# Optimization experiments

Measured on AMD Instinct MI355X. Metric: run time of the kernel, lower is better.

## Reference

```python
import jax, jax.numpy as jnp
import numpy as np

IN_F = 2
DIM_H = 64
DT = 0.02          # step_size
INTENSITY = 40.0   # Poisson rate multiplier
RATE = jnp.array([10.0, 1.0], dtype=jnp.float32)  # Gamma rates per feature


def _xavier(key, fan_in, fan_out):
    lim = float(np.sqrt(6.0 / (fan_in + fan_out)))
    return jax.random.uniform(key, (fan_in, fan_out), minval=-lim, maxval=lim, dtype=jnp.float32)


def setup_inputs() -> dict:
    key = jax.random.key(0)
    k0, k1, k2 = jax.random.split(key, 3)
    Nsim, steps = 100000, 200
    z0 = jax.random.normal(k0, (Nsim, IN_F), dtype=jnp.float32)
    W1 = _xavier(k1, IN_F, DIM_H)
    b1 = jnp.zeros((DIM_H,), dtype=jnp.float32)
    W2 = _xavier(k2, DIM_H, IN_F)
    b2 = jnp.zeros((IN_F,), dtype=jnp.float32)
    diffusion = jnp.float32(1.0)
    return {"z0": z0, "W1": W1, "b1": b1, "W2": W2, "b2": b2,
            "diffusion": diffusion, "Nsim": Nsim, "steps": steps}


def _drift(x, W1, b1, W2, b2):
    # MLP: Linear(2,64) -> tanh -> Linear(64,2)
    h = jnp.tanh(x @ W1 + b1)
    return h @ W2 + b2


def reference(z0, W1, b1, W2, b2, diffusion, Nsim, steps):
    sqrt_dt = jnp.float32(np.sqrt(DT))
    n = z0.shape[0]

    def step(state, key):
        kp, kn, kg = jax.random.split(key, 3)
        # Poisson(intensity*dt) jump counts, shape [N,1]
        pois = jax.random.poisson(kp, INTENSITY * DT, (n, 1)).astype(jnp.float32)
        a = jnp.broadcast_to(pois, (n, IN_F))  # Gamma concentration per feature
        # Gamma(conc=pois, rate=RATE); conc==0 -> sample is exactly 0
        g = jax.random.gamma(kg, jnp.maximum(a, 1.0), dtype=jnp.float32) / RATE
        jump = jnp.where(a > 0, g, 0.0)
        noise = jax.random.normal(kn, (n, IN_F), dtype=jnp.float32)
        new_state = (state
                     + _drift(state, W1, b1, W2, b2) * DT
                     + diffusion * sqrt_dt * noise
                     + jump)
        return new_state, new_state

    keys = jax.random.split(jax.random.key(42), steps)
    _, path = jax.lax.scan(step, z0, keys)            # [steps, N, F]
    path = jnp.concatenate([z0[None], path], axis=0)   # [steps+1, N, F]
    return jnp.transpose(path, (1, 0, 2))              # [N, steps+1, F]
```

## Files before the change

kernel.cpp:

```cpp
#include <hip/hip_runtime.h>
#include <cstdint>
#include <cmath>

#define DEVINL __device__ __forceinline__

struct U2 { uint32_t a, b; };
typedef float v2f __attribute__((ext_vector_type(2)));

DEVINL uint32_t rotl32(uint32_t x, uint32_t r){ return (x << r) | (x >> (32u - r)); }

DEVINL U2 tf(uint32_t k0, uint32_t k1, uint32_t x0, uint32_t x1){
  const uint32_t k2 = k0 ^ k1 ^ 0x1BD11BDAu;
  x0 += k0; x1 += k1;
#define TFR(r) { x0 += x1; x1 = rotl32(x1,(r)); x1 ^= x0; }
  TFR(13) TFR(15) TFR(26) TFR(6)  x0 += k1; x1 += k2 + 1u;
  TFR(17) TFR(29) TFR(16) TFR(24) x0 += k2; x1 += k0 + 2u;
  TFR(13) TFR(15) TFR(26) TFR(6)  x0 += k0; x1 += k1 + 3u;
  TFR(17) TFR(29) TFR(16) TFR(24) x0 += k1; x1 += k2 + 4u;
  TFR(13) TFR(15) TFR(26) TFR(6)  x0 += k2; x1 += k0 + 5u;
#undef TFR
  U2 r; r.a = x0; r.b = x1; return r;
}

DEVINL uint32_t pbits(uint32_t k0, uint32_t k1, uint32_t idx){
  U2 r = tf(k0, k1, 0u, idx);
  return r.a ^ r.b;
}

DEVINL float u01(uint32_t bits){
  return __uint_as_float((bits >> 9) | 0x3F800000u) - 1.0f;
}

DEVINL float xla_logf(float xin){
  float xf = fmaxf(__uint_as_float(0x00800000u), xin);
  uint32_t ib = __float_as_uint(xf);
  float e = (float)((int)(ib >> 23) - 126);
  float x = __uint_as_float((ib & 0x807fffffu) | 0x3f000000u);
  bool m = x < 0.707106781186547524f;
  float t = m ? x : 0.0f;
  x = __fsub_rn(x, 1.0f);
  if (m) e = __fsub_rn(e, 1.0f);
  x = __fadd_rn(x, t);
  float z = __fmul_rn(x, x);
  float y = 7.0376836292e-2f;
  y = fmaf(y, x, -1.1514610310e-1f);
  y = fmaf(y, x,  1.1676998740e-1f);
  y = fmaf(y, x, -1.2420140846e-1f);
  y = fmaf(y, x,  1.4249322787e-1f);
  y = fmaf(y, x, -1.6668057665e-1f);
  y = fmaf(y, x,  2.0000714765e-1f);
  y = fmaf(y, x, -2.4999993993e-1f);
  y = fmaf(y, x,  3.3333331174e-1f);
  y = __fmul_rn(y, x);
  y = __fmul_rn(y, z);
  y = fmaf(e, -2.12194440e-4f, y);
  y = fmaf(z, -0.5f, y);
  x = __fadd_rn(x, y);
  x = fmaf(e, 0.693359375f, x);
  if (xin == 0.0f) x = __uint_as_float(0xff800000u);
  return x;
}

DEVINL float xla_log1pf(float v){
  float av = fabsf(v);
  if (av < 1e-4f) return __fmul_rn(__fadd_rn(__fmul_rn(-0.5f, v), 1.0f), v);
  return xla_logf(__fadd_rn(v, 1.0f));
}

DEVINL float erfinv32(float x){
  float xx = __fmul_rn(x, x);
  float w = -xla_log1pf(-xx);
  float p;
  if (w < 5.0f){
    float ww = __fsub_rn(w, 2.5f);
    p = 2.81022636e-08f;
    p = __fadd_rn( 3.43273939e-07f, __fmul_rn(p, ww));
    p = __fadd_rn(-3.5233877e-06f,  __fmul_rn(p, ww));
    p = __fadd_rn(-4.39150654e-06f, __fmul_rn(p, ww));
    p = __fadd_rn( 0.00021858087f,  __fmul_rn(p, ww));
    p = __fadd_rn(-0.00125372503f,  __fmul_rn(p, ww));
    p = __fadd_rn(-0.00417768164f,  __fmul_rn(p, ww));
    p = __fadd_rn( 0.246640727f,    __fmul_rn(p, ww));
    p = __fadd_rn( 1.50140941f,     __fmul_rn(p, ww));
  } else {
    float ww = __fsub_rn(sqrtf(w), 3.0f);
    p = -0.000200214257f;
    p = __fadd_rn( 0.000100950558f, __fmul_rn(p, ww));
    p = __fadd_rn( 0.00134934322f,  __fmul_rn(p, ww));
    p = __fadd_rn(-0.00367342844f,  __fmul_rn(p, ww));
    p = __fadd_rn( 0.00573950773f,  __fmul_rn(p, ww));
    p = __fadd_rn(-0.0076224613f,   __fmul_rn(p, ww));
    p = __fadd_rn( 0.00943887047f,  __fmul_rn(p, ww));
    p = __fadd_rn( 1.00167406f,     __fmul_rn(p, ww));
    p = __fadd_rn( 2.83297682f,     __fmul_rn(p, ww));
  }
  return __fmul_rn(p, x);
}

#define SQRT2F (__uint_as_float(0x3FB504F3u))
#define NLOF   (__uint_as_float(0xBF7FFFFFu))
#define SQDTF  ((float)0.14142135623730951)

DEVINL float normal_from_bits(uint32_t bits){
  float ff = u01(bits);
  float u = __fadd_rn(__fmul_rn(ff, 2.0f), NLOF);
  u = fmaxf(NLOF, u);
  return __fmul_rn(SQRT2F, erfinv32(u));
}

DEVINL float fast_tanh(float x){
  float ax = fabsf(x);
  float e = __expf(-2.0f * ax);
  float r = (1.0f - e) * __builtin_amdgcn_rcpf(1.0f + e);
  return __builtin_copysignf(r, x);
}

DEVINL v2f f2fma(v2f a, v2f b, v2f c){ return __builtin_elementwise_fma(a, b, c); }

DEVINL float gamma_one(uint32_t gk0, uint32_t gk1, float alpha){
  const float d = __fsub_rn(alpha, (1.0f/3.0f));
  const float c = (1.0f/3.0f) / sqrtf(d);
  U2 K = tf(gk0, gk1, 0u, 0u);
  for (;;) {
    U2 xk = tf(K.a, K.b, 0u, 1u);
    U2 Uk = tf(K.a, K.b, 0u, 2u);
    float xx, v;
    for (;;) {
      U2 sub = tf(xk.a, xk.b, 0u, 1u);
      uint32_t nb = pbits(sub.a, sub.b, 0u);
      xx = normal_from_bits(nb);
      v = __fadd_rn(1.0f, __fmul_rn(xx, c));
      if (v > 0.0f) break;
      xk = tf(xk.a, xk.b, 0u, 0u);
    }
    float X = __fmul_rn(xx, xx);
    float V = __fmul_rn(__fmul_rn(v, v), v);
    float U = u01(pbits(Uk.a, Uk.b, 0u));
    float sq = __fsub_rn(1.0f, __fmul_rn(0.0331f, __fmul_rn(X, X)));
    if (U < sq) return __fmul_rn(d, V);
    float lnU = xla_logf(U);
    float lnV = xla_logf(V);
    float rhs = __fadd_rn(__fmul_rn(X, 0.5f),
                          __fmul_rn(d, __fadd_rn(__fsub_rn(1.0f, V), lnV)));
    if (lnU < rhs) return __fmul_rn(d, V);
    K = tf(K.a, K.b, 0u, 0u);
  }
}

#define NPK 24
#define WSTRIDE (4 + 2*NPK)
#define KEYOFF 8
#define JOFF   16384

__global__ void setup_kernel(uint32_t* __restrict__ ws, int steps){
  int t = blockIdx.x * blockDim.x + threadIdx.x;
  if (t >= steps) return;
  U2 kt = tf(0u, 42u, 0u, (uint32_t)t);
  U2 kp = tf(kt.a, kt.b, 0u, 0u);
  U2 kn = tf(kt.a, kt.b, 0u, 1u);
  U2 kg = tf(kt.a, kt.b, 0u, 2u);
  uint32_t* p = ws + KEYOFF + (size_t)t * WSTRIDE;
  p[0] = kn.a; p[1] = kn.b;
  p[2] = kg.a; p[3] = kg.b;
  uint32_t r0 = kp.a, r1 = kp.b;
  for (int i = 0; i < NPK; ++i) {
    U2 sub = tf(r0, r1, 0u, 1u);
    U2 rn  = tf(r0, r1, 0u, 0u);
    p[4 + 2*i] = sub.a; p[5 + 2*i] = sub.b;
    r0 = rn.a; r1 = rn.b;
  }
}

#define PEL 4
__global__ __launch_bounds__(64) void pois_kernel(
    uint32_t* __restrict__ ws, const float* __restrict__ diffp,
    int N, int steps, uint32_t POFF, uint32_t COFF)
{
  const int lane = threadIdx.x;
  const int t = blockIdx.y;
  const int base = blockIdx.x * (64 * PEL);
  const uint32_t* __restrict__ p = ws + KEYOFF + (size_t)t * WSTRIDE;
  const float coef = __fmul_rn(diffp[0], SQDTF);

  int poisv[PEL];
  #pragma unroll
  for (int j = 0; j < PEL; ++j) poisv[j] = -1;

  int cur = 0;
  int e = base + lane;
  float lp = 0.0f; int k = 0;
  bool done = (e >= N);

  #pragma unroll 1
  for (int guard = 0; guard < PEL * NPK + PEL + 1; ++guard) {
    if (!__any(!done)) break;
    if (!done) {
      if (!(lp > -0.8f)) {
        poisv[cur] = k - 1;
        cur++;
        lp = 0.0f; k = 0;
        int ne = base + cur * 64 + lane;
        if (cur >= PEL || ne >= N) done = true;
        else e = ne;
      }
    }
    if (!done) {
      uint32_t bits = pbits(p[4 + 2*k], p[5 + 2*k], (uint32_t)e);
      lp = __fadd_rn(lp, xla_logf(u01(bits)));
      k++;
      if (k >= NPK) lp = -1.0f;
    }
  }

  float* jarr = (float*)(ws + JOFF);
  uint8_t* pb = (uint8_t*)ws + (size_t)POFF * 4u + (size_t)t * (size_t)N;
  const uint32_t kn0 = p[0], kn1 = p[1];
  int mycnt = 0;
  #pragma unroll
  for (int j = 0; j < PEL; ++j) {
    int ej = base + j * 64 + lane;
    if (ej < N) {
      pb[ej] = (uint8_t)poisv[j];
      float nf0 = normal_from_bits(pbits(kn0, kn1, 2u*(uint32_t)ej));
      float nf1 = normal_from_bits(pbits(kn0, kn1, 2u*(uint32_t)ej + 1u));
      size_t jb = (size_t)t * (size_t)(2*N) + 2u * (uint32_t)ej;
      jarr[jb]     = __fmul_rn(coef, nf0);
      jarr[jb + 1] = __fmul_rn(coef, nf1);
      if (poisv[j] > 0) mycnt++;
    }
  }
  int c = mycnt;
  #pragma unroll
  for (int off = 32; off > 0; off >>= 1) c += __shfl_xor(c, off, 64);
  if (lane == 0)
    ws[COFF + (size_t)t * gridDim.x + blockIdx.x] = (uint32_t)c;
}

__global__ __launch_bounds__(256) void prefix_kernel(
    uint32_t* __restrict__ ws, uint32_t COFF, uint32_t BOFF, int NB)
{
  __shared__ uint32_t ssum[256];
  int i = threadIdx.x;
  int chunk = (NB + 255) >> 8;
  int lo = i * chunk, hi = lo + chunk; if (hi > NB) hi = NB;
  uint32_t s = 0;
  for (int j = lo; j < hi; ++j) s += ws[COFF + j];
  ssum[i] = s;
  __syncthreads();
  if (i == 0) {
    uint32_t run = 0;
    for (int k = 0; k < 256; ++k) { uint32_t c = ssum[k]; ssum[k] = run; run += c; }
    ws[0] = run;
  }
  __syncthreads();
  uint32_t base = ssum[i];
  for (int j = lo; j < hi; ++j) { ws[BOFF + j] = base; base += ws[COFF + j]; }
}

__global__ __launch_bounds__(256) void scatter_kernel(
    uint32_t* __restrict__ ws, int N, int steps,
    uint32_t POFF, uint32_t BOFF, uint32_t WOFF, uint32_t CAP)
{
  __shared__ uint32_t cnts[4];
  int e = blockIdx.x * 256 + threadIdx.x;
  int t = blockIdx.y;
  bool act = e < N;
  uint32_t pv = 0;
  if (act) pv = ((const uint8_t*)ws)[(size_t)POFF*4u + (size_t)t*(size_t)N + (size_t)e];
  uint64_t b = __ballot(pv > 0);
  int lane = threadIdx.x & 63, w = threadIdx.x >> 6;
  if (lane == 0) cnts[w] = (uint32_t)__popcll(b);
  __syncthreads();
  uint32_t bid = (uint32_t)blockIdx.y * gridDim.x + blockIdx.x;
  uint32_t wb = ws[BOFF + bid];
  for (int w2 = 0; w2 < w; ++w2) wb += cnts[w2];
  if (pv > 0) {
    uint32_t rank = (uint32_t)__popcll(b & ((1ull << lane) - 1ull));
    uint32_t idx = wb + rank;
    if (idx < CAP)
      ws[WOFF + idx] = ((uint32_t)t << 23) | ((uint32_t)e << 6) | pv;
  }
}

__global__ __launch_bounds__(256) void gamma_kernel(
    uint32_t* __restrict__ ws, int N, uint32_t WOFF, uint32_t CAP)
{
  uint32_t total = ws[0]; if (total > CAP) total = CAP;
  uint32_t j = blockIdx.x * 256u + threadIdx.x;
  if (j >= total) return;
  uint32_t ent = ws[WOFF + j];
  uint32_t t = ent >> 23, e = (ent >> 6) & 0x1FFFFu, pv = ent & 0x3Fu;
  const uint32_t* __restrict__ p = ws + KEYOFF + (size_t)t * WSTRIDE;
  uint32_t kg0 = p[2], kg1 = p[3];
  float alpha = (float)pv;
  U2 gka = tf(kg0, kg1, 0u, 2u*e);
  float s0 = gamma_one(gka.a, gka.b, alpha) / 10.0f;
  U2 gkb = tf(kg0, kg1, 0u, 2u*e + 1u);
  float s1 = gamma_one(gkb.a, gkb.b, alpha);
  float* jarr = (float*)(ws + JOFF);
  float2* slot = (float2*)&jarr[(size_t)t * (size_t)(2*N) + (size_t)(2u*e)];
  float2 v = *slot;
  v.x = __fadd_rn(v.x, s0);
  v.y = __fadd_rn(v.y, s1);
  *slot = v;
}

__global__ __launch_bounds__(256) void jump_kernel(
    uint32_t* __restrict__ ws, const float* __restrict__ diffp, int N, int steps)
{
  int e = blockIdx.x * 256 + threadIdx.x;
  int t = blockIdx.y;
  if (e >= N) return;
  const uint32_t* __restrict__ p = ws + KEYOFF + (size_t)t * WSTRIDE;
  const uint32_t ue = (uint32_t)e;
  const float coef = __fmul_rn(diffp[0], SQDTF);
  float lp = 0.0f; int k = 0;
  #pragma unroll 1
  for (int i = 0; i < NPK; ++i) {
    if (!(lp > -0.8f)) break;
    k++;
    uint32_t bits = pbits(p[4 + 2*i], p[5 + 2*i], ue);
    lp = __fadd_rn(lp, xla_logf(u01(bits)));
  }
  int pois = k - 1;
  float nf0 = normal_from_bits(pbits(p[0], p[1], 2u*ue));
  float nf1 = normal_from_bits(pbits(p[0], p[1], 2u*ue + 1u));
  float j0 = __fmul_rn(coef, nf0), j1 = __fmul_rn(coef, nf1);
  if (pois > 0) {
    uint32_t kg0 = p[2], kg1 = p[3];
    float alpha = (float)pois;
    U2 gk0 = tf(kg0, kg1, 0u, 2u*ue);
    j0 = __fadd_rn(j0, gamma_one(gk0.a, gk0.b, alpha) / 10.0f);
    U2 gk1 = tf(kg0, kg1, 0u, 2u*ue + 1u);
    j1 = __fadd_rn(j1, gamma_one(gk1.a, gk1.b, alpha));
  }
  float* jarr = (float*)(ws + JOFF);
  size_t jbase = (size_t)t * (size_t)(2*N) + (size_t)(2*e);
  jarr[jbase] = j0; jarr[jbase + 1] = j1;
}

#define IBLK 256
__global__ __launch_bounds__(IBLK) void integrate_kernel(
    const float* __restrict__ z0, const float* __restrict__ W1,
    const float* __restrict__ b1, const float* __restrict__ W2,
    const float* __restrict__ b2, const float* __restrict__ diffp,
    const uint32_t* __restrict__ ws, float* __restrict__ out,
    int N, int steps)
{
  __shared__ float smem[322];
  for (int k = threadIdx.x; k < 322; k += IBLK) {
    float v;
    if (k < 128)      v = W1[k];
    else if (k < 192) v = b1[k - 128];
    else if (k < 320) v = W2[k - 192];
    else              v = b2[k - 320];
    smem[k] = v;
  }
  __syncthreads();
  const float* sW1 = smem;
  const float* sb1 = smem + 128;
  const float* sW2 = smem + 192;
  const float* sb2 = smem + 320;

  int tid = blockIdx.x * IBLK + threadIdx.x;
  const int e = tid >> 2;
  const int s = tid & 3;
  if (e >= N) return;

  float2 xv = *(const float2*)&z0[2*e];
  float x0 = xv.x, x1 = xv.y;
  const size_t orow = (size_t)(steps + 1) * 2u;
  float* op = out + (size_t)e * orow;
  if (s == 0) *(float2*)&op[0] = xv;

  const float DTf  = 0.02f;
  const int   hbase = s << 4;
  const float2* __restrict__ jarr2 = (const float2*)(ws + JOFF);
  const float b20 = sb2[0], b21 = sb2[1];

  for (int t = 0; t < steps; ++t) {
    float2 S = jarr2[(size_t)t * (size_t)N + (size_t)e];

    v2f xv0 = (v2f){x0, x0};
    v2f xv1 = (v2f){x1, x1};
    v2f acc = (v2f){0.0f, 0.0f};
    #pragma unroll
    for (int j = 0; j < 8; ++j) {
      int h = hbase + 2*j;
      v2f w1lo = *(const v2f*)&sW1[h];
      v2f w1hi = *(const v2f*)&sW1[64 + h];
      v2f b1v  = *(const v2f*)&sb1[h];
      v2f pre  = f2fma(xv0, w1lo, f2fma(xv1, w1hi, b1v));
      float hv0 = fast_tanh(pre.x);
      float hv1 = fast_tanh(pre.y);
      v2f w2a = *(const v2f*)&sW2[2*h];
      v2f w2b = *(const v2f*)&sW2[2*h + 2];
      acc = f2fma((v2f){hv0, hv0}, w2a, acc);
      acc = f2fma((v2f){hv1, hv1}, w2b, acc);
    }
    float q0 = acc.x, q1 = acc.y;
    q0 = q0 + __shfl_xor(q0, 1, 64);
    q1 = q1 + __shfl_xor(q1, 1, 64);
    q0 = q0 + __shfl_xor(q0, 2, 64);
    q1 = q1 + __shfl_xor(q1, 2, 64);
    float dr0 = b20 + q0;
    float dr1 = b21 + q1;

    x0 = __fadd_rn(__fadd_rn(x0, __fmul_rn(dr0, DTf)), S.x);
    x1 = __fadd_rn(__fadd_rn(x1, __fmul_rn(dr1, DTf)), S.y);
    if (s == 0) {
      float2 o; o.x = x0; o.y = x1;
      *(float2*)&op[(size_t)(t + 1) * 2u] = o;
    }
  }
}

__global__ __launch_bounds__(64) void sim_fallback_kernel(
    const float* __restrict__ z0, const float* __restrict__ W1,
    const float* __restrict__ b1, const float* __restrict__ W2,
    const float* __restrict__ b2, const float* __restrict__ diffp,
    const uint32_t* __restrict__ ws, float* __restrict__ out,
    int N, int steps)
{
  __shared__ float smem[322];
  for (int k = threadIdx.x; k < 322; k += 64) {
    float v;
    if (k < 128)      v = W1[k];
    else if (k < 192) v = b1[k - 128];
    else if (k < 320) v = W2[k - 192];
    else              v = b2[k - 320];
    smem[k] = v;
  }
  __syncthreads();
  const float* sW1 = smem;
  const float* sb1 = smem + 128;
  const float* sW2 = smem + 192;
  const float* sb2 = smem + 320;

  int tid = blockIdx.x * 64 + threadIdx.x;
  if (tid >= 2 * N) return;
  const int e = tid >> 1;
  const int f = tid & 1;
  const uint32_t ue   = (uint32_t)e;
  const uint32_t utid = (uint32_t)tid;

  float x = z0[tid];
  const size_t obase = (size_t)e * (size_t)(steps + 1) * 2u + (size_t)f;
  out[obase] = x;

  const float DTf  = 0.02f;
  const float coef = __fmul_rn(diffp[0], SQDTF);
  const int   hbase = f << 5;

  for (int t = 0; t < steps; ++t) {
    const uint32_t* __restrict__ p = ws + KEYOFF + (size_t)t * WSTRIDE;
    int pois;
    {
      float lp = 0.0f;
      pois = NPK - 1;
      #pragma unroll 1
      for (int m = 0; m < NPK/2; ++m) {
        int i0 = 2*m + f;
        uint32_t bits = pbits(p[4 + 2*i0], p[5 + 2*i0], ue);
        float lmine = xla_logf(u01(bits));
        float lother = __shfl_xor(lmine, 1, 64);
        float la = (f == 0) ? lmine : lother;
        float lb = (f == 0) ? lother : lmine;
        float s1 = __fadd_rn(lp, la);
        float s2 = __fadd_rn(s1, lb);
        if (!(s1 > -0.8f)) { pois = 2*m; break; }
        if (!(s2 > -0.8f)) { pois = 2*m + 1; break; }
        lp = s2;
      }
    }
    float nf = normal_from_bits(pbits(p[0], p[1], utid));
    float jump = 0.0f;
    if (pois > 0) {
      U2 gk = tf(p[2], p[3], 0u, utid);
      float s = gamma_one(gk.a, gk.b, (float)pois);
      jump = (f == 0) ? (s / 10.0f) : s;
    }
    float xo = __shfl_xor(x, 1, 64);
    float xf0 = (f == 0) ? x : xo;
    float xf1 = (f == 0) ? xo : x;
    float p0 = 0.0f, p1 = 0.0f;
    #pragma unroll
    for (int i = 0; i < 32; ++i) {
      int h = hbase + i;
      float hv = fast_tanh(fmaf(xf0, sW1[h], fmaf(xf1, sW1[64 + h], sb1[h])));
      p0 = fmaf(hv, sW2[2*h],     p0);
      p1 = fmaf(hv, sW2[2*h + 1], p1);
    }
    float q0 = p0 + __shfl_xor(p0, 1, 64);
    float q1 = p1 + __shfl_xor(p1, 1, 64);
    float dr = sb2[f] + ((f == 0) ? q0 : q1);
    x = __fadd_rn(__fadd_rn(__fadd_rn(x, __fmul_rn(dr, DTf)),
                            __fmul_rn(coef, nf)), jump);
    out[obase + (size_t)(t + 1) * 2u] = x;
  }
}

extern "C" void kernel_launch(void* const* d_in, const int* in_sizes, int n_in,
                              void* d_out, int out_size, void* d_ws, size_t ws_size,
                              hipStream_t stream) {
  const float* z0  = (const float*)d_in[0];
  const float* W1  = (const float*)d_in[1];
  const float* b1  = (const float*)d_in[2];
  const float* W2  = (const float*)d_in[3];
  const float* b2  = (const float*)d_in[4];
  const float* dif = (const float*)d_in[5];
  int N = in_sizes[0] / 2;
  int steps = out_size / (N * 2) - 1;
  uint32_t* ws = (uint32_t*)d_ws;
  int total = 2 * N;

  hipLaunchKernelGGL(setup_kernel, dim3((steps + 255) / 256), dim3(256), 0, stream,
                     ws, steps);

  size_t JSZ = (size_t)2 * (size_t)N * (size_t)steps;
  size_t PSZ = ((size_t)N * (size_t)steps + 3u) / 4u;
  int    NBX = (N + 255) / 256;
  size_t NB  = (size_t)NBX * (size_t)steps;
  size_t CAP = ((size_t)N * (size_t)steps * 11u) / 16u;
  size_t POFFs = (size_t)JOFF + JSZ;
  size_t COFFs = POFFs + PSZ;
  size_t BOFFs = COFFs + NB;
  size_t WOFFs = BOFFs + NB;
  size_t need0 = (WOFFs + CAP) * 4u;
  size_t need1 = ((size_t)JOFF + JSZ) * 4u;
  bool pk = (N < (1 << 17)) && (steps < (1 << 9)) && (steps <= 314) &&
            (WOFFs + CAP < 0xFFFFFFFFull);

  int total4 = 4 * N;

  if (pk && ws_size >= need0) {
    hipLaunchKernelGGL(pois_kernel, dim3(NBX, steps), dim3(64), 0, stream,
                       ws, dif, N, steps, (uint32_t)POFFs, (uint32_t)COFFs);
    hipLaunchKernelGGL(prefix_kernel, dim3(1), dim3(256), 0, stream,
                       ws, (uint32_t)COFFs, (uint32_t)BOFFs, (int)NB);
    hipLaunchKernelGGL(scatter_kernel, dim3(NBX, steps), dim3(256), 0, stream,
                       ws, N, steps, (uint32_t)POFFs, (uint32_t)BOFFs,
                       (uint32_t)WOFFs, (uint32_t)CAP);
    hipLaunchKernelGGL(gamma_kernel, dim3((CAP + 255) / 256), dim3(256), 0, stream,
                       ws, N, (uint32_t)WOFFs, (uint32_t)CAP);
    hipLaunchKernelGGL(integrate_kernel, dim3((total4 + IBLK - 1) / IBLK), dim3(IBLK),
                       0, stream, z0, W1, b1, W2, b2, dif, ws, (float*)d_out, N, steps);
  } else if (steps <= 314 && ws_size >= need1) {
    hipLaunchKernelGGL(jump_kernel, dim3((N + 255) / 256, steps), dim3(256), 0, stream,
                       ws, dif, N, steps);
    hipLaunchKernelGGL(integrate_kernel, dim3((total4 + IBLK - 1) / IBLK), dim3(IBLK),
                       0, stream, z0, W1, b1, W2, b2, dif, ws, (float*)d_out, N, steps);
  } else {
    hipLaunchKernelGGL(sim_fallback_kernel, dim3((total + 63) / 64), dim3(64), 0, stream,
                       z0, W1, b1, W2, b2, dif, ws, (float*)d_out, N, steps);
  }
}
```

Baseline: 1.542 ms.

## Split gamma rejection sampling into single-attempt pass plus compacted retry pass

```diff
diff --git a/kernel.cpp b/kernel.cpp
--- a/kernel.cpp
+++ b/kernel.cpp
@@ -117,34 +117,44 @@
 
 DEVINL v2f f2fma(v2f a, v2f b, v2f c){ return __builtin_elementwise_fma(a, b, c); }
 
-DEVINL float gamma_one(uint32_t gk0, uint32_t gk1, float alpha){
+DEVINL bool gamma_attempt(uint32_t K0, uint32_t K1, float d, float c, float& out){
+  U2 xk = tf(K0, K1, 0u, 1u);
+  U2 Uk = tf(K0, K1, 0u, 2u);
+  float xx, v;
+  for (;;) {
+    U2 sub = tf(xk.a, xk.b, 0u, 1u);
+    xx = normal_from_bits(pbits(sub.a, sub.b, 0u));
+    v = __fadd_rn(1.0f, __fmul_rn(xx, c));
+    if (v > 0.0f) break;
+    xk = tf(xk.a, xk.b, 0u, 0u);
+  }
+  float X = __fmul_rn(xx, xx);
+  float V = __fmul_rn(__fmul_rn(v, v), v);
+  float U = u01(pbits(Uk.a, Uk.b, 0u));
+  float sq = __fsub_rn(1.0f, __fmul_rn(0.0331f, __fmul_rn(X, X)));
+  if (U < sq) { out = __fmul_rn(d, V); return true; }
+  float lnU = xla_logf(U);
+  float lnV = xla_logf(V);
+  float rhs = __fadd_rn(__fmul_rn(X, 0.5f),
+                        __fmul_rn(d, __fadd_rn(__fsub_rn(1.0f, V), lnV)));
+  if (lnU < rhs) { out = __fmul_rn(d, V); return true; }
+  return false;
+}
+
+DEVINL float gamma_fromK(uint32_t K0, uint32_t K1, float alpha){
   const float d = __fsub_rn(alpha, (1.0f/3.0f));
   const float c = (1.0f/3.0f) / sqrtf(d);
+  for (;;) {
+    float s;
+    if (gamma_attempt(K0, K1, d, c, s)) return s;
+    U2 K = tf(K0, K1, 0u, 0u);
+    K0 = K.a; K1 = K.b;
+  }
+}
+
+DEVINL float gamma_one(uint32_t gk0, uint32_t gk1, float alpha){
   U2 K = tf(gk0, gk1, 0u, 0u);
-  for (;;) {
-    U2 xk = tf(K.a, K.b, 0u, 1u);
-    U2 Uk = tf(K.a, K.b, 0u, 2u);
-    float xx, v;
-    for (;;) {
-      U2 sub = tf(xk.a, xk.b, 0u, 1u);
-      uint32_t nb = pbits(sub.a, sub.b, 0u);
-      xx = normal_from_bits(nb);
-      v = __fadd_rn(1.0f, __fmul_rn(xx, c));
-      if (v > 0.0f) break;
-      xk = tf(xk.a, xk.b, 0u, 0u);
-    }
-    float X = __fmul_rn(xx, xx);
-    float V = __fmul_rn(__fmul_rn(v, v), v);
-    float U = u01(pbits(Uk.a, Uk.b, 0u));
-    float sq = __fsub_rn(1.0f, __fmul_rn(0.0331f, __fmul_rn(X, X)));
-    if (U < sq) return __fmul_rn(d, V);
-    float lnU = xla_logf(U);
-    float lnV = xla_logf(V);
-    float rhs = __fadd_rn(__fmul_rn(X, 0.5f),
-                          __fmul_rn(d, __fadd_rn(__fsub_rn(1.0f, V), lnV)));
-    if (lnU < rhs) return __fmul_rn(d, V);
-    K = tf(K.a, K.b, 0u, 0u);
-  }
+  return gamma_fromK(K.a, K.b, alpha);
 }
 
 #define NPK 24
@@ -237,7 +247,7 @@
 }
 
 __global__ __launch_bounds__(256) void prefix_kernel(
-    uint32_t* __restrict__ ws, uint32_t COFF, uint32_t BOFF, int NB)
+    uint32_t* __restrict__ ws, uint32_t COFF, uint32_t BOFF, int NB, int outIdx)
 {
   __shared__ uint32_t ssum[256];
   int i = threadIdx.x;
@@ -250,7 +260,7 @@
   if (i == 0) {
     uint32_t run = 0;
     for (int k = 0; k < 256; ++k) { uint32_t c = ssum[k]; ssum[k] = run; run += c; }
-    ws[0] = run;
+    ws[outIdx] = run;
   }
   __syncthreads();
   uint32_t base = ssum[i];
@@ -282,27 +292,106 @@
   }
 }
 
-__global__ __launch_bounds__(256) void gamma_kernel(
-    uint32_t* __restrict__ ws, int N, uint32_t WOFF, uint32_t CAP)
-{
+__global__ __launch_bounds__(256) void gamma_pass1(
+    uint32_t* __restrict__ ws, int N,
+    uint32_t WOFF, uint32_t CAP, uint32_t FOFF, uint32_t COFF)
+{
+  __shared__ uint32_t cnts[4];
   uint32_t total = ws[0]; if (total > CAP) total = CAP;
   uint32_t j = blockIdx.x * 256u + threadIdx.x;
-  if (j >= total) return;
+  uint32_t fb = 0;
+  if (j < total) {
+    uint32_t ent = ws[WOFF + j];
+    uint32_t t = ent >> 23, e = (ent >> 6) & 0x1FFFFu, pv = ent & 0x3Fu;
+    const uint32_t* __restrict__ p = ws + KEYOFF + (size_t)t * WSTRIDE;
+    uint32_t kg0 = p[2], kg1 = p[3];
+    float alpha = (float)pv;
+    const float d = __fsub_rn(alpha, (1.0f/3.0f));
+    const float c = (1.0f/3.0f) / sqrtf(d);
+    float add0 = 0.0f, add1 = 0.0f;
+    {
+      U2 gk = tf(kg0, kg1, 0u, 2u*e);
+      U2 K  = tf(gk.a, gk.b, 0u, 0u);
+      float s;
+      if (gamma_attempt(K.a, K.b, d, c, s)) add0 = s / 10.0f; else fb |= 1u;
+    }
+    {
+      U2 gk = tf(kg0, kg1, 0u, 2u*e + 1u);
+      U2 K  = tf(gk.a, gk.b, 0u, 0u);
+      float s;
+      if (gamma_attempt(K.a, K.b, d, c, s)) add1 = s; else fb |= 2u;
+    }
+    float* jarr = (float*)(ws + JOFF);
+    float2* slot = (float2*)&jarr[(size_t)t * (size_t)(2*N) + (size_t)(2u*e)];
+    float2 v = *slot;
+    v.x = __fadd_rn(v.x, add0);
+    v.y = __fadd_rn(v.y, add1);
+    *slot = v;
+  }
+  if (j < CAP) ((uint8_t*)ws)[(size_t)FOFF*4u + j] = (uint8_t)fb;
+  uint64_t b = __ballot(fb != 0u);
+  int lane = threadIdx.x & 63, w = threadIdx.x >> 6;
+  if (lane == 0) cnts[w] = (uint32_t)__popcll(b);
+  __syncthreads();
+  if (threadIdx.x == 0)
+    ws[COFF + blockIdx.x] = cnts[0] + cnts[1] + cnts[2] + cnts[3];
+}
+
+__global__ __launch_bounds__(256) void retry_scatter(
+    uint32_t* __restrict__ ws, uint32_t FOFF, uint32_t BOFF,
+    uint32_t WOFF, uint32_t CAP)
+{
+  __shared__ uint32_t cnts[4];
+  uint32_t totalA = ws[0]; if (totalA > CAP) totalA = CAP;
+  uint32_t spare = CAP - totalA;
+  uint32_t j = blockIdx.x * 256u + threadIdx.x;
+  uint32_t fb = 0;
+  if (j < CAP) fb = ((const uint8_t*)ws)[(size_t)FOFF*4u + j];
+  uint64_t b = __ballot(fb != 0u);
+  int lane = threadIdx.x & 63, w = threadIdx.x >> 6;
+  if (lane == 0) cnts[w] = (uint32_t)__popcll(b);
+  __syncthreads();
+  uint32_t wb = ws[BOFF + blockIdx.x];
+  for (int w2 = 0; w2 < w; ++w2) wb += cnts[w2];
+  if (fb != 0u) {
+    uint32_t rank = (uint32_t)__popcll(b & ((1ull << lane) - 1ull));
+    uint32_t idx = wb + rank;
+    if (idx < spare) ws[WOFF + totalA + idx] = (j << 2) | fb;
+  }
+}
+
+__global__ __launch_bounds__(256) void retry_exec(
+    uint32_t* __restrict__ ws, int N, uint32_t WOFF, uint32_t CAP, uint32_t RMAX)
+{
+  uint32_t totalA = ws[0]; if (totalA > CAP) totalA = CAP;
+  uint32_t spare = CAP - totalA;
+  uint32_t rtot = ws[1];
+  if (rtot > spare) rtot = spare;
+  if (rtot > RMAX) rtot = RMAX;
+  uint32_t i = blockIdx.x * 256u + threadIdx.x;
+  if (i >= rtot) return;
+  uint32_t rec = ws[WOFF + totalA + i];
+  uint32_t j = rec >> 2, fb = rec & 3u;
   uint32_t ent = ws[WOFF + j];
   uint32_t t = ent >> 23, e = (ent >> 6) & 0x1FFFFu, pv = ent & 0x3Fu;
   const uint32_t* __restrict__ p = ws + KEYOFF + (size_t)t * WSTRIDE;
-  uint32_t kg0 = p[2], kg1 = p[3];
   float alpha = (float)pv;
-  U2 gka = tf(kg0, kg1, 0u, 2u*e);
-  float s0 = gamma_one(gka.a, gka.b, alpha) / 10.0f;
-  U2 gkb = tf(kg0, kg1, 0u, 2u*e + 1u);
-  float s1 = gamma_one(gkb.a, gkb.b, alpha);
   float* jarr = (float*)(ws + JOFF);
-  float2* slot = (float2*)&jarr[(size_t)t * (size_t)(2*N) + (size_t)(2u*e)];
-  float2 v = *slot;
-  v.x = __fadd_rn(v.x, s0);
-  v.y = __fadd_rn(v.y, s1);
-  *slot = v;
+  size_t jb = (size_t)t * (size_t)(2*N) + (size_t)(2u*e);
+  if (fb & 1u) {
+    U2 gk = tf(p[2], p[3], 0u, 2u*e);
+    U2 K  = tf(gk.a, gk.b, 0u, 0u);
+    K = tf(K.a, K.b, 0u, 0u);
+    float s = gamma_fromK(K.a, K.b, alpha) / 10.0f;
+    jarr[jb] = __fadd_rn(jarr[jb], s);
+  }
+  if (fb & 2u) {
+    U2 gk = tf(p[2], p[3], 0u, 2u*e + 1u);
+    U2 K  = tf(gk.a, gk.b, 0u, 0u);
+    K = tf(K.a, K.b, 0u, 0u);
+    float s = gamma_fromK(K.a, K.b, alpha);
+    jarr[jb + 1] = __fadd_rn(jarr[jb + 1], s);
+  }
 }
 
 __global__ __launch_bounds__(256) void jump_kernel(
@@ -528,8 +617,9 @@
   size_t WOFFs = BOFFs + NB;
   size_t need0 = (WOFFs + CAP) * 4u;
   size_t need1 = ((size_t)JOFF + JSZ) * 4u;
+  int    NB2 = (int)((CAP + 255u) / 256u);
   bool pk = (N < (1 << 17)) && (steps < (1 << 9)) && (steps <= 314) &&
-            (WOFFs + CAP < 0xFFFFFFFFull);
+            ((size_t)NB2 <= NB) && (WOFFs + CAP < 0xFFFFFFFFull);
 
   int total4 = 4 * N;
 
@@ -537,12 +627,21 @@
     hipLaunchKernelGGL(pois_kernel, dim3(NBX, steps), dim3(64), 0, stream,
                        ws, dif, N, steps, (uint32_t)POFFs, (uint32_t)COFFs);
     hipLaunchKernelGGL(prefix_kernel, dim3(1), dim3(256), 0, stream,
-                       ws, (uint32_t)COFFs, (uint32_t)BOFFs, (int)NB);
+                       ws, (uint32_t)COFFs, (uint32_t)BOFFs, (int)NB, 0);
     hipLaunchKernelGGL(scatter_kernel, dim3(NBX, steps), dim3(256), 0, stream,
                        ws, N, steps, (uint32_t)POFFs, (uint32_t)BOFFs,
                        (uint32_t)WOFFs, (uint32_t)CAP);
-    hipLaunchKernelGGL(gamma_kernel, dim3((CAP + 255) / 256), dim3(256), 0, stream,
-                       ws, N, (uint32_t)WOFFs, (uint32_t)CAP);
+    hipLaunchKernelGGL(gamma_pass1, dim3(NB2), dim3(256), 0, stream,
+                       ws, N, (uint32_t)WOFFs, (uint32_t)CAP,
+                       (uint32_t)POFFs, (uint32_t)COFFs);
+    hipLaunchKernelGGL(prefix_kernel, dim3(1), dim3(256), 0, stream,
+                       ws, (uint32_t)COFFs, (uint32_t)BOFFs, NB2, 1);
+    hipLaunchKernelGGL(retry_scatter, dim3(NB2), dim3(256), 0, stream,
+                       ws, (uint32_t)POFFs, (uint32_t)BOFFs,
+                       (uint32_t)WOFFs, (uint32_t)CAP);
+    uint32_t RMAX = (uint32_t)(((CAP / 4u) + 255u) / 256u) * 256u;
+    hipLaunchKernelGGL(retry_exec, dim3(RMAX / 256u), dim3(256), 0, stream,
+                       ws, N, (uint32_t)WOFFs, (uint32_t)CAP, RMAX);
     hipLaunchKernelGGL(integrate_kernel, dim3((total4 + IBLK - 1) / IBLK), dim3(IBLK),
                        0, stream, z0, W1, b1, W2, b2, dif, ws, (float*)d_out, N, steps);
   } else if (steps <= 314 && ws_size >= need1) {
```

New measurement: 1.472 ms. -4.6%, faster.
